# Optimization experiments

Hardware: AMD Instinct MI355X
Metric: run time of the kernel (lower is better)

## Reference

```python
import jax, jax.numpy as jnp
import numpy as np

N = 50000      # nodes
E = 800000     # edges in normalized A (incl. self loops)
DIN = 128      # input_dim
DOUT = 64      # output_dim
BN_EPS = 1e-5
SLOPE = 0.01   # LeakyReLU default negative slope


def setup_inputs() -> dict:
    key = jax.random.key(0)
    ks = jax.random.split(key, 10)
    H = jax.random.normal(ks[0], (N, DIN), dtype=jnp.float32)
    rows = jax.random.randint(ks[1], (E,), 0, N, dtype=jnp.int32)
    cols = jax.random.randint(ks[2], (E,), 0, N, dtype=jnp.int32)
    # values of the symmetrically normalized adjacency (precomputed in __init__)
    vals = jax.random.uniform(ks[3], (E,), dtype=jnp.float32)
    # BatchNorm1d params/buffers (eval mode: use running stats)
    gamma = 1.0 + 0.1 * jax.random.normal(ks[4], (DIN,), dtype=jnp.float32)
    beta = 0.1 * jax.random.normal(ks[5], (DIN,), dtype=jnp.float32)
    run_mean = 0.1 * jax.random.normal(ks[6], (DIN,), dtype=jnp.float32)
    run_var = 0.5 + jax.random.uniform(ks[7], (DIN,), dtype=jnp.float32)
    # Linear(input_dim, output_dim)
    W = jax.random.normal(ks[8], (DIN, DOUT), dtype=jnp.float32) / np.sqrt(DIN)
    b = 0.01 * jax.random.normal(ks[9], (DOUT,), dtype=jnp.float32)
    return dict(H=H, rows=rows, cols=cols, vals=vals, gamma=gamma, beta=beta,
                run_mean=run_mean, run_var=run_var, W=W, b=b)


def reference(H, rows, cols, vals, gamma, beta, run_mean, run_var, W, b):
    # F.normalize: L2 row normalization with eps=1e-12
    norm = jnp.maximum(jnp.linalg.norm(H, axis=1, keepdims=True), 1e-12)
    Hn = H / norm
    # BatchNorm1d (eval: running stats); dropout is identity in eval
    scale = gamma * jax.lax.rsqrt(run_var + BN_EPS)
    Hb = (Hn - run_mean) * scale + beta
    # Linear projection [N, DIN] @ [DIN, DOUT]
    X = Hb @ W + b
    # SpMM: out[r] = sum_{e: rows[e]==r} vals[e] * X[cols[e]]
    msgs = vals[:, None] * X[cols]            # [E, DOUT] gather + scale
    out = jax.ops.segment_sum(msgs, rows, num_segments=N)
    # LeakyReLU
    return jnp.where(out >= 0, out, SLOPE * out)
```

## Files before the change

### kernel.cpp

```cpp
#include <hip/hip_runtime.h>
#include <hip/hip_fp16.h>

#define N_NODES 50000
#define E_EDGES 800000
#define DIN 128
#define DOUT 64
#define NBUK 196
#define BUKCAP 4608
#define CHUNK 2048
#define NBLKA 391
#define NGRP 1563
#define GCAP 704
#define ASTRIDE 136

typedef short short8 __attribute__((ext_vector_type(8)));
typedef float f32x4 __attribute__((ext_vector_type(4)));

static __device__ __forceinline__ short f2bf(float f)
{
    union { float f; unsigned u; } x{f};
    const unsigned r = x.u + 0x7FFFu + ((x.u >> 16) & 1u);
    return (short)(r >> 16);
}

__global__ __launch_bounds__(256) void k_x(
    const float* __restrict__ H, const float* __restrict__ gamma,
    const float* __restrict__ beta, const float* __restrict__ mean,
    const float* __restrict__ var, const float* __restrict__ W,
    const float* __restrict__ bias, unsigned short* __restrict__ X16,
    int* __restrict__ gcursor)
{
    __shared__ short A_s[64][ASTRIDE];
    __shared__ short B_s[64][ASTRIDE];
    const int t = threadIdx.x;
    const int l = t & 63, wv = t >> 6;
    const int R0 = blockIdx.x * 64;

    if (blockIdx.x == 0 && t < NBUK) gcursor[t] = 0;

    {
        const int n = t >> 2, koff = (t & 3) * 32;
#pragma unroll
        for (int i = 0; i < 16; ++i) {
            const int k = koff + i * 2;
            const unsigned lo = (unsigned short)f2bf(W[k * DOUT + n]);
            const unsigned hi = (unsigned short)f2bf(W[(k + 1) * DOUT + n]);
            *(unsigned*)&B_s[n][k] = lo | (hi << 16);
        }
    }
    {
        const int rloc = t >> 2, sub = t & 3;
        const int r = R0 + rloc;
        float4 h[8];
        if (r < N_NODES) {
            const float4* hp = (const float4*)(H + (size_t)r * DIN + sub * 32);
#pragma unroll
            for (int i = 0; i < 8; ++i) h[i] = hp[i];
        } else {
#pragma unroll
            for (int i = 0; i < 8; ++i) h[i] = make_float4(0.f, 0.f, 0.f, 0.f);
        }
        float ss = 0.f;
#pragma unroll
        for (int i = 0; i < 8; ++i)
            ss += h[i].x * h[i].x + h[i].y * h[i].y + h[i].z * h[i].z + h[i].w * h[i].w;
        ss += __shfl_xor(ss, 1, 64);
        ss += __shfl_xor(ss, 2, 64);
        const float inv = 1.0f / fmaxf(sqrtf(ss), 1e-12f);

        const float4* gp = (const float4*)(gamma + sub * 32);
        const float4* bp = (const float4*)(beta  + sub * 32);
        const float4* mp = (const float4*)(mean  + sub * 32);
        const float4* vp = (const float4*)(var   + sub * 32);
#pragma unroll
        for (int i = 0; i < 8; ++i) {
            const float4 g4 = gp[i], b4 = bp[i], m4 = mp[i], v4 = vp[i];
            const float s0 = g4.x * rsqrtf(v4.x + 1e-5f);
            const float s1 = g4.y * rsqrtf(v4.y + 1e-5f);
            const float s2 = g4.z * rsqrtf(v4.z + 1e-5f);
            const float s3 = g4.w * rsqrtf(v4.w + 1e-5f);
            const float e0 = h[i].x * inv * s0 + (b4.x - m4.x * s0);
            const float e1 = h[i].y * inv * s1 + (b4.y - m4.y * s1);
            const float e2 = h[i].z * inv * s2 + (b4.z - m4.z * s2);
            const float e3 = h[i].w * inv * s3 + (b4.w - m4.w * s3);
            const unsigned u0 = (unsigned short)f2bf(e0) | ((unsigned)(unsigned short)f2bf(e1) << 16);
            const unsigned u1 = (unsigned short)f2bf(e2) | ((unsigned)(unsigned short)f2bf(e3) << 16);
            *(uint2*)&A_s[rloc][sub * 32 + i * 4] = make_uint2(u0, u1);
        }
    }

    const int ml = l & 15, q = l >> 4;
    f32x4 c0, c1, c2, c3;
    {
        const float b0 = bias[ml],      b1 = bias[16 + ml];
        const float b2 = bias[32 + ml], b3 = bias[48 + ml];
        c0 = f32x4{b0, b0, b0, b0};
        c1 = f32x4{b1, b1, b1, b1};
        c2 = f32x4{b2, b2, b2, b2};
        c3 = f32x4{b3, b3, b3, b3};
    }
    __syncthreads();

#pragma unroll
    for (int k0 = 0; k0 < 4; ++k0) {
        const short8 a  = *(const short8*)&A_s[wv * 16 + ml][k0 * 32 + q * 8];
        const short8 b0 = *(const short8*)&B_s[ml][k0 * 32 + q * 8];
        const short8 b1 = *(const short8*)&B_s[16 + ml][k0 * 32 + q * 8];
        const short8 b2 = *(const short8*)&B_s[32 + ml][k0 * 32 + q * 8];
        const short8 b3 = *(const short8*)&B_s[48 + ml][k0 * 32 + q * 8];
        c0 = __builtin_amdgcn_mfma_f32_16x16x32_bf16(a, b0, c0, 0, 0, 0);
        c1 = __builtin_amdgcn_mfma_f32_16x16x32_bf16(a, b1, c1, 0, 0, 0);
        c2 = __builtin_amdgcn_mfma_f32_16x16x32_bf16(a, b2, c2, 0, 0, 0);
        c3 = __builtin_amdgcn_mfma_f32_16x16x32_bf16(a, b3, c3, 0, 0, 0);
    }

    __syncthreads();
    unsigned short* otile = (unsigned short*)&A_s[0][0];
#pragma unroll
    for (int i = 0; i < 4; ++i) {
        const int r = wv * 16 + q * 4 + i;
        otile[r * 64 + ml]      = __half_as_ushort(__float2half(c0[i]));
        otile[r * 64 + 16 + ml] = __half_as_ushort(__float2half(c1[i]));
        otile[r * 64 + 32 + ml] = __half_as_ushort(__float2half(c2[i]));
        otile[r * 64 + 48 + ml] = __half_as_ushort(__float2half(c3[i]));
    }
    __syncthreads();
#pragma unroll
    for (int rep = 0; rep < 2; ++rep) {
        const int id = rep * 256 + t;
        const int row = id >> 3;
        const int off = (id & 7) * 8;
        if (R0 + row < N_NODES)
            *(uint4*)(X16 + (size_t)(R0 + row) * DOUT + off) =
                *(const uint4*)&otile[row * 64 + off];
    }
}

__global__ __launch_bounds__(512) void k_passA(
    const int* __restrict__ rows, const int* __restrict__ cols,
    const float* __restrict__ vals, int* __restrict__ gcursor,
    unsigned* __restrict__ midVC, unsigned char* __restrict__ midR)
{
    __shared__ int lhist[NBUK], lstart[NBUK], lcur[NBUK], gbase[NBUK];
    __shared__ int wsumS[4];
    __shared__ unsigned lbinVC[CHUNK];
    __shared__ unsigned short lbinBR[CHUNK];
    const int t = threadIdx.x;
    const int lane = t & 63, wv = t >> 6;
    const int e0 = blockIdx.x * CHUNK;
    const int nC = min(CHUNK, E_EDGES - e0);

    if (t < NBUK) lhist[t] = 0;
    __syncthreads();

    unsigned prVC[4];
    unsigned short prBR[4];
#pragma unroll
    for (int k = 0; k < 4; ++k) {
        const int e = e0 + k * 512 + t;
        if (e < E_EDGES) {
            const int r = rows[e];
            const unsigned hv = __half_as_ushort(__float2half(vals[e]));
            prVC[k] = (hv << 16) | (unsigned)cols[e];
            prBR[k] = (unsigned short)r;
            atomicAdd(&lhist[r >> 8], 1);
        } else {
            prBR[k] = 0xFFFFu;
        }
    }
    __syncthreads();

    const int v = (t < NBUK) ? lhist[t] : 0;
    int x = v;
    if (t < 256) {
#pragma unroll
        for (int o = 1; o < 64; o <<= 1) {
            const int y = __shfl_up(x, o, 64);
            if (lane >= o) x += y;
        }
        if (lane == 63) wsumS[wv] = x;
    }
    __syncthreads();
    if (t < NBUK) {
        int pre = 0;
        for (int i = 0; i < wv; ++i) pre += wsumS[i];
        const int ex = pre + x - v;
        lstart[t] = ex;
        lcur[t] = ex;
        gbase[t] = t * BUKCAP + (v ? atomicAdd(&gcursor[t], v) : 0);
    }
    __syncthreads();

#pragma unroll
    for (int k = 0; k < 4; ++k) {
        if (prBR[k] != 0xFFFFu) {
            const int bk = prBR[k] >> 8;
            const int pos = atomicAdd(&lcur[bk], 1);
            lbinVC[pos] = prVC[k];
            lbinBR[pos] = prBR[k];
        }
    }
    __syncthreads();

    for (int i = t; i < nC; i += 512) {
        const unsigned short br = lbinBR[i];
        const int bk = br >> 8;
        const int g = gbase[bk] + (i - lstart[bk]);
        if (g < (bk + 1) * BUKCAP) {
            midVC[g] = lbinVC[i];
            midR[g] = (unsigned char)(br & 255);
        }
    }
}

__global__ __launch_bounds__(256) void k_passB(
    const int* __restrict__ gcursor, const unsigned* __restrict__ midVC,
    const unsigned char* __restrict__ midR, unsigned* __restrict__ ev,
    int2* __restrict__ rowSE)
{
    __shared__ int lhist[32], lcur[32];
    const int g  = blockIdx.x;
    const int bk = g >> 3;
    const int q  = g & 7;
    const int base = bk * BUKCAP;
    const int total = min(gcursor[bk], BUKCAP);
    const int t = threadIdx.x;

    if (t < 32) lhist[t] = 0;
    __syncthreads();
    for (int i = t; i < total; i += 256) {
        const int lr = midR[base + i];
        if ((lr >> 5) == q) atomicAdd(&lhist[lr & 31], 1);
    }
    __syncthreads();
    if (t < 32) {
        const int v = lhist[t];
        int x = v;
#pragma unroll
        for (int o = 1; o < 32; o <<= 1) {
            const int y = __shfl_up(x, o, 64);
            if (t >= o) x += y;
        }
        const int ex = x - v;
        lcur[t] = min(ex, GCAP);
        const int row = (g << 5) | t;
        if (row < N_NODES)
            rowSE[row] = make_int2(g * GCAP + min(ex, GCAP),
                                   g * GCAP + min(ex + v, GCAP));
    }
    __syncthreads();
    for (int i = t; i < total; i += 256) {
        const int lr = midR[base + i];
        if ((lr >> 5) == q) {
            const int pos = atomicAdd(&lcur[lr & 31], 1);
            if (pos < GCAP) ev[g * GCAP + pos] = midVC[base + i];
        }
    }
}

__global__ __launch_bounds__(256) void k_spmm(
    const int2* __restrict__ rowSE, const unsigned* __restrict__ ev,
    const unsigned short* __restrict__ X16, float* __restrict__ out)
{
    const int lane = threadIdx.x & 63;
    const int ql   = lane & 15;
    const int qh   = lane >> 4;
    const int row  = blockIdx.x * 4 + (threadIdx.x >> 6);
    const int2 se = rowSE[row];
    const int s = se.x, e2 = se.y;
    float a0 = 0.f, a1 = 0.f, a2 = 0.f, a3 = 0.f;
    for (int c = s; c < e2; c += 64) {
        const int idx = c + lane;
        unsigned p = 0;
        if (idx < e2) p = ev[idx];
        const int cnt  = min(e2 - c, 64);
        const int jmax = (cnt + 3) >> 2;
        int j = 0;
        for (; j + 1 < jmax; j += 2) {
            const unsigned u0 = (unsigned)__shfl((int)p, 4 * j + qh,     64);
            const unsigned u1 = (unsigned)__shfl((int)p, 4 * j + 4 + qh, 64);
            const uint2 x0 = *(const uint2*)(X16 + (u0 & 0xFFFFu) * DOUT + 4 * ql);
            const uint2 x1 = *(const uint2*)(X16 + (u1 & 0xFFFFu) * DOUT + 4 * ql);
            const float v0 = __half2float(__ushort_as_half((unsigned short)(u0 >> 16)));
            const float v1 = __half2float(__ushort_as_half((unsigned short)(u1 >> 16)));
            const float2 f00 = __half22float2(*(const __half2*)&x0.x);
            const float2 f01 = __half22float2(*(const __half2*)&x0.y);
            const float2 f10 = __half22float2(*(const __half2*)&x1.x);
            const float2 f11 = __half22float2(*(const __half2*)&x1.y);
            a0 = fmaf(v0, f00.x, a0); a1 = fmaf(v0, f00.y, a1);
            a2 = fmaf(v0, f01.x, a2); a3 = fmaf(v0, f01.y, a3);
            a0 = fmaf(v1, f10.x, a0); a1 = fmaf(v1, f10.y, a1);
            a2 = fmaf(v1, f11.x, a2); a3 = fmaf(v1, f11.y, a3);
        }
        for (; j < jmax; ++j) {
            const unsigned u = (unsigned)__shfl((int)p, 4 * j + qh, 64);
            const uint2 xx = *(const uint2*)(X16 + (u & 0xFFFFu) * DOUT + 4 * ql);
            const float v = __half2float(__ushort_as_half((unsigned short)(u >> 16)));
            const float2 f0 = __half22float2(*(const __half2*)&xx.x);
            const float2 f1 = __half22float2(*(const __half2*)&xx.y);
            a0 = fmaf(v, f0.x, a0); a1 = fmaf(v, f0.y, a1);
            a2 = fmaf(v, f1.x, a2); a3 = fmaf(v, f1.y, a3);
        }
    }
    a0 += __shfl_xor(a0, 16, 64); a0 += __shfl_xor(a0, 32, 64);
    a1 += __shfl_xor(a1, 16, 64); a1 += __shfl_xor(a1, 32, 64);
    a2 += __shfl_xor(a2, 16, 64); a2 += __shfl_xor(a2, 32, 64);
    a3 += __shfl_xor(a3, 16, 64); a3 += __shfl_xor(a3, 32, 64);
    if (lane < 16) {
        float4 r;
        r.x = (a0 >= 0.f) ? a0 : 0.01f * a0;
        r.y = (a1 >= 0.f) ? a1 : 0.01f * a1;
        r.z = (a2 >= 0.f) ? a2 : 0.01f * a2;
        r.w = (a3 >= 0.f) ? a3 : 0.01f * a3;
        *(float4*)(out + (size_t)row * DOUT + 4 * ql) = r;
    }
}

extern "C" void kernel_launch(void* const* d_in, const int* in_sizes, int n_in,
                              void* d_out, int out_size, void* d_ws, size_t ws_size,
                              hipStream_t stream)
{
    const float* H     = (const float*)d_in[0];
    const int*   rows  = (const int*)  d_in[1];
    const int*   cols  = (const int*)  d_in[2];
    const float* vals  = (const float*)d_in[3];
    const float* gamma = (const float*)d_in[4];
    const float* beta  = (const float*)d_in[5];
    const float* mean  = (const float*)d_in[6];
    const float* var   = (const float*)d_in[7];
    const float* W     = (const float*)d_in[8];
    const float* bias  = (const float*)d_in[9];
    float* out = (float*)d_out;

    char* ws = (char*)d_ws;
    unsigned short* X16     = (unsigned short*)(ws);
    int*            gcursor = (int*)          (ws +  6400000);
    unsigned*       midVC   = (unsigned*)     (ws +  6400800);
    unsigned char*  midR    = (unsigned char*)(ws + 10013472);
    unsigned*       ev      = (unsigned*)     (ws + 10916640);
    int2*           rowSE   = (int2*)         (ws + 15318048);

    k_x<<<(N_NODES + 63) / 64, 256, 0, stream>>>(H, gamma, beta, mean, var, W,
                                                 bias, X16, gcursor);
    k_passA<<<NBLKA, 512, 0, stream>>>(rows, cols, vals, gcursor, midVC, midR);
    k_passB<<<NGRP, 256, 0, stream>>>(gcursor, midVC, midR, ev, rowSE);
    k_spmm<<<N_NODES / 4, 256, 0, stream>>>(rowSE, ev, X16, out);
}
```

Measured before the change: 160.6 us.

## Fuse row-bucketing pass with SpMM using LDS atomic accumulation per 32-row group

Replaces the second bucketing pass and the per-row SpMM kernel with one kernel per 32-row group. Each group compacts its matching edges into shared memory with a wave-ballot queue, then gathers X rows and accumulates with shared-memory float atomics into a padded 32x64 tile. LeakyReLU is applied when the tile is written out. This removes one launch and the global round trip through the ev and rowSE buffers. In exchange it relies on LDS atomics, whose contention may be high, and float summation order is no longer deterministic.

```diff
diff --git a/kernel.cpp b/kernel.cpp
--- a/kernel.cpp
+++ b/kernel.cpp
@@ -10,7 +10,7 @@
 #define CHUNK 2048
 #define NBLKA 391
 #define NGRP 1563
-#define GCAP 704
+#define QCAP 768
 #define ASTRIDE 136
 
 typedef short short8 __attribute__((ext_vector_type(8)));
@@ -213,106 +213,76 @@
     }
 }
 
-__global__ __launch_bounds__(256) void k_passB(
+__global__ __launch_bounds__(256) void k_spmmf(
     const int* __restrict__ gcursor, const unsigned* __restrict__ midVC,
-    const unsigned char* __restrict__ midR, unsigned* __restrict__ ev,
-    int2* __restrict__ rowSE)
-{
-    __shared__ int lhist[32], lcur[32];
-    const int g  = blockIdx.x;
+    const unsigned char* __restrict__ midR, const unsigned short* __restrict__ X16,
+    float* __restrict__ out)
+{
+    __shared__ float acc[32 * 65];
+    __shared__ unsigned qVC[QCAP];
+    __shared__ int qR[QCAP];
+    __shared__ int qcount;
+    const int t = threadIdx.x;
+    const int g = blockIdx.x;
     const int bk = g >> 3;
     const int q  = g & 7;
     const int base = bk * BUKCAP;
     const int total = min(gcursor[bk], BUKCAP);
-    const int t = threadIdx.x;
-
-    if (t < 32) lhist[t] = 0;
-    __syncthreads();
-    for (int i = t; i < total; i += 256) {
-        const int lr = midR[base + i];
-        if ((lr >> 5) == q) atomicAdd(&lhist[lr & 31], 1);
-    }
-    __syncthreads();
-    if (t < 32) {
-        const int v = lhist[t];
-        int x = v;
-#pragma unroll
-        for (int o = 1; o < 32; o <<= 1) {
-            const int y = __shfl_up(x, o, 64);
-            if (t >= o) x += y;
-        }
-        const int ex = x - v;
-        lcur[t] = min(ex, GCAP);
-        const int row = (g << 5) | t;
-        if (row < N_NODES)
-            rowSE[row] = make_int2(g * GCAP + min(ex, GCAP),
-                                   g * GCAP + min(ex + v, GCAP));
-    }
-    __syncthreads();
-    for (int i = t; i < total; i += 256) {
-        const int lr = midR[base + i];
-        if ((lr >> 5) == q) {
-            const int pos = atomicAdd(&lcur[lr & 31], 1);
-            if (pos < GCAP) ev[g * GCAP + pos] = midVC[base + i];
-        }
-    }
-}
-
-__global__ __launch_bounds__(256) void k_spmm(
-    const int2* __restrict__ rowSE, const unsigned* __restrict__ ev,
-    const unsigned short* __restrict__ X16, float* __restrict__ out)
-{
-    const int lane = threadIdx.x & 63;
-    const int ql   = lane & 15;
-    const int qh   = lane >> 4;
-    const int row  = blockIdx.x * 4 + (threadIdx.x >> 6);
-    const int2 se = rowSE[row];
-    const int s = se.x, e2 = se.y;
-    float a0 = 0.f, a1 = 0.f, a2 = 0.f, a3 = 0.f;
-    for (int c = s; c < e2; c += 64) {
-        const int idx = c + lane;
-        unsigned p = 0;
-        if (idx < e2) p = ev[idx];
-        const int cnt  = min(e2 - c, 64);
-        const int jmax = (cnt + 3) >> 2;
-        int j = 0;
-        for (; j + 1 < jmax; j += 2) {
-            const unsigned u0 = (unsigned)__shfl((int)p, 4 * j + qh,     64);
-            const unsigned u1 = (unsigned)__shfl((int)p, 4 * j + 4 + qh, 64);
-            const uint2 x0 = *(const uint2*)(X16 + (u0 & 0xFFFFu) * DOUT + 4 * ql);
-            const uint2 x1 = *(const uint2*)(X16 + (u1 & 0xFFFFu) * DOUT + 4 * ql);
-            const float v0 = __half2float(__ushort_as_half((unsigned short)(u0 >> 16)));
-            const float v1 = __half2float(__ushort_as_half((unsigned short)(u1 >> 16)));
-            const float2 f00 = __half22float2(*(const __half2*)&x0.x);
-            const float2 f01 = __half22float2(*(const __half2*)&x0.y);
-            const float2 f10 = __half22float2(*(const __half2*)&x1.x);
-            const float2 f11 = __half22float2(*(const __half2*)&x1.y);
-            a0 = fmaf(v0, f00.x, a0); a1 = fmaf(v0, f00.y, a1);
-            a2 = fmaf(v0, f01.x, a2); a3 = fmaf(v0, f01.y, a3);
-            a0 = fmaf(v1, f10.x, a0); a1 = fmaf(v1, f10.y, a1);
-            a2 = fmaf(v1, f11.x, a2); a3 = fmaf(v1, f11.y, a3);
-        }
-        for (; j < jmax; ++j) {
-            const unsigned u = (unsigned)__shfl((int)p, 4 * j + qh, 64);
-            const uint2 xx = *(const uint2*)(X16 + (u & 0xFFFFu) * DOUT + 4 * ql);
-            const float v = __half2float(__ushort_as_half((unsigned short)(u >> 16)));
-            const float2 f0 = __half22float2(*(const __half2*)&xx.x);
-            const float2 f1 = __half22float2(*(const __half2*)&xx.y);
-            a0 = fmaf(v, f0.x, a0); a1 = fmaf(v, f0.y, a1);
-            a2 = fmaf(v, f1.x, a2); a3 = fmaf(v, f1.y, a3);
-        }
-    }
-    a0 += __shfl_xor(a0, 16, 64); a0 += __shfl_xor(a0, 32, 64);
-    a1 += __shfl_xor(a1, 16, 64); a1 += __shfl_xor(a1, 32, 64);
-    a2 += __shfl_xor(a2, 16, 64); a2 += __shfl_xor(a2, 32, 64);
-    a3 += __shfl_xor(a3, 16, 64); a3 += __shfl_xor(a3, 32, 64);
-    if (lane < 16) {
-        float4 r;
-        r.x = (a0 >= 0.f) ? a0 : 0.01f * a0;
-        r.y = (a1 >= 0.f) ? a1 : 0.01f * a1;
-        r.z = (a2 >= 0.f) ? a2 : 0.01f * a2;
-        r.w = (a3 >= 0.f) ? a3 : 0.01f * a3;
-        *(float4*)(out + (size_t)row * DOUT + 4 * ql) = r;
+    const int lane = t & 63;
+
+    for (int i = t; i < 32 * 65; i += 256) acc[i] = 0.f;
+    if (t == 0) qcount = 0;
+    __syncthreads();
+
+    for (int i0 = t; i0 < total; i0 += 256) {
+        const int lr = midR[base + i0];
+        const bool match = (lr >> 5) == q;
+        const unsigned long long m = __ballot(match);
+        if (m) {
+            const int ldr = (int)(__ffsll((long long)m) - 1);
+            const int pre = __popcll(m & ((1ull << lane) - 1ull));
+            int bs = 0;
+            if (lane == ldr) bs = atomicAdd(&qcount, __popcll(m));
+            bs = __shfl(bs, ldr, 64);
+            if (match) {
+                const int pos = bs + pre;
+                if (pos < QCAP) {
+                    qVC[pos] = midVC[base + i0];
+                    qR[pos]  = lr & 31;
+                }
+            }
+        }
+    }
+    __syncthreads();
+    const int qc = min(qcount, QCAP);
+
+    const int grp = t >> 4;
+    const int ql  = t & 15;
+    for (int i = grp; i < qc; i += 16) {
+        const unsigned vc = qVC[i];
+        const int rl = qR[i];
+        const float v = __half2float(__ushort_as_half((unsigned short)(vc >> 16)));
+        const uint2 x = *(const uint2*)(X16 + (size_t)(vc & 0xFFFFu) * DOUT + 4 * ql);
+        const float2 f0 = __half22float2(*(const __half2*)&x.x);
+        const float2 f1 = __half22float2(*(const __half2*)&x.y);
+        float* ap = &acc[rl * 65 + 4 * ql];
+        atomicAdd(ap + 0, v * f0.x);
+        atomicAdd(ap + 1, v * f0.y);
+        atomicAdd(ap + 2, v * f1.x);
+        atomicAdd(ap + 3, v * f1.y);
+    }
+    __syncthreads();
+
+    const int r0 = g << 5;
+#pragma unroll
+    for (int k = 0; k < 8; ++k) {
+        const int id = k * 256 + t;
+        const int r = id >> 6, c = id & 63;
+        if (r0 + r < N_NODES) {
+            float a = acc[r * 65 + c];
+            a = (a >= 0.f) ? a : 0.01f * a;
+            out[(size_t)(r0 + r) * DOUT + c] = a;
+        }
     }
 }
 
@@ -337,12 +307,9 @@
     int*            gcursor = (int*)          (ws +  6400000);
     unsigned*       midVC   = (unsigned*)     (ws +  6400800);
     unsigned char*  midR    = (unsigned char*)(ws + 10013472);
-    unsigned*       ev      = (unsigned*)     (ws + 10916640);
-    int2*           rowSE   = (int2*)         (ws + 15318048);
 
     k_x<<<(N_NODES + 63) / 64, 256, 0, stream>>>(H, gamma, beta, mean, var, W,
                                                  bias, X16, gcursor);
     k_passA<<<NBLKA, 512, 0, stream>>>(rows, cols, vals, gcursor, midVC, midR);
-    k_passB<<<NGRP, 256, 0, stream>>>(gcursor, midVC, midR, ev, rowSE);
-    k_spmm<<<N_NODES / 4, 256, 0, stream>>>(rowSE, ev, X16, out);
-}
+    k_spmmf<<<NGRP, 256, 0, stream>>>(gcursor, midVC, midR, X16, out);
+}
```

Result: slower. 434.7 us (+170.6%).

## Merge feature projection and edge binning into one launch; narrow SpMM gather

Applied to the files above, without the earlier changes.

Fuses the dense projection kernel and the first edge-bucketing pass into a single launch. Blocks are dispatched by block index to either role, so the two independent stages run concurrently and one launch is saved. The gcursor reset moves to a hipMemsetAsync, which adds a small operation. Separately, the SpMM kernel now processes two edges per iteration, with 32 lanes each loading 4 bytes, instead of four edges with 16 lanes each loading 8 bytes. This trades load width against the number of shuffle reductions.

```diff
diff --git a/kernel.cpp b/kernel.cpp
--- a/kernel.cpp
+++ b/kernel.cpp
@@ -9,9 +9,11 @@
 #define BUKCAP 4608
 #define CHUNK 2048
 #define NBLKA 391
+#define NXP 391
 #define NGRP 1563
 #define GCAP 704
 #define ASTRIDE 136
+#define TILEB (64 * ASTRIDE * 2)
 
 typedef short short8 __attribute__((ext_vector_type(8)));
 typedef float f32x4 __attribute__((ext_vector_type(4)));
@@ -23,192 +25,197 @@
     return (short)(r >> 16);
 }
 
-__global__ __launch_bounds__(256) void k_x(
+__global__ __launch_bounds__(512) void k_xa(
     const float* __restrict__ H, const float* __restrict__ gamma,
     const float* __restrict__ beta, const float* __restrict__ mean,
     const float* __restrict__ var, const float* __restrict__ W,
     const float* __restrict__ bias, unsigned short* __restrict__ X16,
-    int* __restrict__ gcursor)
-{
-    __shared__ short A_s[64][ASTRIDE];
-    __shared__ short B_s[64][ASTRIDE];
-    const int t = threadIdx.x;
-    const int l = t & 63, wv = t >> 6;
-    const int R0 = blockIdx.x * 64;
-
-    if (blockIdx.x == 0 && t < NBUK) gcursor[t] = 0;
-
-    {
-        const int n = t >> 2, koff = (t & 3) * 32;
-#pragma unroll
-        for (int i = 0; i < 16; ++i) {
-            const int k = koff + i * 2;
-            const unsigned lo = (unsigned short)f2bf(W[k * DOUT + n]);
-            const unsigned hi = (unsigned short)f2bf(W[(k + 1) * DOUT + n]);
-            *(unsigned*)&B_s[n][k] = lo | (hi << 16);
-        }
-    }
-    {
-        const int rloc = t >> 2, sub = t & 3;
-        const int r = R0 + rloc;
-        float4 h[8];
-        if (r < N_NODES) {
-            const float4* hp = (const float4*)(H + (size_t)r * DIN + sub * 32);
-#pragma unroll
-            for (int i = 0; i < 8; ++i) h[i] = hp[i];
-        } else {
-#pragma unroll
-            for (int i = 0; i < 8; ++i) h[i] = make_float4(0.f, 0.f, 0.f, 0.f);
-        }
-        float ss = 0.f;
-#pragma unroll
-        for (int i = 0; i < 8; ++i)
-            ss += h[i].x * h[i].x + h[i].y * h[i].y + h[i].z * h[i].z + h[i].w * h[i].w;
-        ss += __shfl_xor(ss, 1, 64);
-        ss += __shfl_xor(ss, 2, 64);
-        const float inv = 1.0f / fmaxf(sqrtf(ss), 1e-12f);
-
-        const float4* gp = (const float4*)(gamma + sub * 32);
-        const float4* bp = (const float4*)(beta  + sub * 32);
-        const float4* mp = (const float4*)(mean  + sub * 32);
-        const float4* vp = (const float4*)(var   + sub * 32);
-#pragma unroll
-        for (int i = 0; i < 8; ++i) {
-            const float4 g4 = gp[i], b4 = bp[i], m4 = mp[i], v4 = vp[i];
-            const float s0 = g4.x * rsqrtf(v4.x + 1e-5f);
-            const float s1 = g4.y * rsqrtf(v4.y + 1e-5f);
-            const float s2 = g4.z * rsqrtf(v4.z + 1e-5f);
-            const float s3 = g4.w * rsqrtf(v4.w + 1e-5f);
-            const float e0 = h[i].x * inv * s0 + (b4.x - m4.x * s0);
-            const float e1 = h[i].y * inv * s1 + (b4.y - m4.y * s1);
-            const float e2 = h[i].z * inv * s2 + (b4.z - m4.z * s2);
-            const float e3 = h[i].w * inv * s3 + (b4.w - m4.w * s3);
-            const unsigned u0 = (unsigned short)f2bf(e0) | ((unsigned)(unsigned short)f2bf(e1) << 16);
-            const unsigned u1 = (unsigned short)f2bf(e2) | ((unsigned)(unsigned short)f2bf(e3) << 16);
-            *(uint2*)&A_s[rloc][sub * 32 + i * 4] = make_uint2(u0, u1);
-        }
-    }
-
-    const int ml = l & 15, q = l >> 4;
-    f32x4 c0, c1, c2, c3;
-    {
-        const float b0 = bias[ml],      b1 = bias[16 + ml];
-        const float b2 = bias[32 + ml], b3 = bias[48 + ml];
-        c0 = f32x4{b0, b0, b0, b0};
-        c1 = f32x4{b1, b1, b1, b1};
-        c2 = f32x4{b2, b2, b2, b2};
-        c3 = f32x4{b3, b3, b3, b3};
-    }
-    __syncthreads();
-
-#pragma unroll
-    for (int k0 = 0; k0 < 4; ++k0) {
-        const short8 a  = *(const short8*)&A_s[wv * 16 + ml][k0 * 32 + q * 8];
-        const short8 b0 = *(const short8*)&B_s[ml][k0 * 32 + q * 8];
-        const short8 b1 = *(const short8*)&B_s[16 + ml][k0 * 32 + q * 8];
-        const short8 b2 = *(const short8*)&B_s[32 + ml][k0 * 32 + q * 8];
-        const short8 b3 = *(const short8*)&B_s[48 + ml][k0 * 32 + q * 8];
-        c0 = __builtin_amdgcn_mfma_f32_16x16x32_bf16(a, b0, c0, 0, 0, 0);
-        c1 = __builtin_amdgcn_mfma_f32_16x16x32_bf16(a, b1, c1, 0, 0, 0);
-        c2 = __builtin_amdgcn_mfma_f32_16x16x32_bf16(a, b2, c2, 0, 0, 0);
-        c3 = __builtin_amdgcn_mfma_f32_16x16x32_bf16(a, b3, c3, 0, 0, 0);
-    }
-
-    __syncthreads();
-    unsigned short* otile = (unsigned short*)&A_s[0][0];
-#pragma unroll
-    for (int i = 0; i < 4; ++i) {
-        const int r = wv * 16 + q * 4 + i;
-        otile[r * 64 + ml]      = __half_as_ushort(__float2half(c0[i]));
-        otile[r * 64 + 16 + ml] = __half_as_ushort(__float2half(c1[i]));
-        otile[r * 64 + 32 + ml] = __half_as_ushort(__float2half(c2[i]));
-        otile[r * 64 + 48 + ml] = __half_as_ushort(__float2half(c3[i]));
-    }
-    __syncthreads();
-#pragma unroll
-    for (int rep = 0; rep < 2; ++rep) {
-        const int id = rep * 256 + t;
-        const int row = id >> 3;
-        const int off = (id & 7) * 8;
-        if (R0 + row < N_NODES)
-            *(uint4*)(X16 + (size_t)(R0 + row) * DOUT + off) =
-                *(const uint4*)&otile[row * 64 + off];
-    }
-}
-
-__global__ __launch_bounds__(512) void k_passA(
     const int* __restrict__ rows, const int* __restrict__ cols,
     const float* __restrict__ vals, int* __restrict__ gcursor,
     unsigned* __restrict__ midVC, unsigned char* __restrict__ midR)
 {
-    __shared__ int lhist[NBUK], lstart[NBUK], lcur[NBUK], gbase[NBUK];
-    __shared__ int wsumS[4];
-    __shared__ unsigned lbinVC[CHUNK];
-    __shared__ unsigned short lbinBR[CHUNK];
+    __shared__ __align__(16) char smem[2][TILEB * 2];
+    const int bid = blockIdx.x;
     const int t = threadIdx.x;
-    const int lane = t & 63, wv = t >> 6;
-    const int e0 = blockIdx.x * CHUNK;
-    const int nC = min(CHUNK, E_EDGES - e0);
-
-    if (t < NBUK) lhist[t] = 0;
-    __syncthreads();
-
-    unsigned prVC[4];
-    unsigned short prBR[4];
-#pragma unroll
-    for (int k = 0; k < 4; ++k) {
-        const int e = e0 + k * 512 + t;
-        if (e < E_EDGES) {
-            const int r = rows[e];
-            const unsigned hv = __half_as_ushort(__float2half(vals[e]));
-            prVC[k] = (hv << 16) | (unsigned)cols[e];
-            prBR[k] = (unsigned short)r;
-            atomicAdd(&lhist[r >> 8], 1);
-        } else {
-            prBR[k] = 0xFFFFu;
-        }
-    }
-    __syncthreads();
-
-    const int v = (t < NBUK) ? lhist[t] : 0;
-    int x = v;
-    if (t < 256) {
-#pragma unroll
-        for (int o = 1; o < 64; o <<= 1) {
-            const int y = __shfl_up(x, o, 64);
-            if (lane >= o) x += y;
-        }
-        if (lane == 63) wsumS[wv] = x;
-    }
-    __syncthreads();
-    if (t < NBUK) {
-        int pre = 0;
-        for (int i = 0; i < wv; ++i) pre += wsumS[i];
-        const int ex = pre + x - v;
-        lstart[t] = ex;
-        lcur[t] = ex;
-        gbase[t] = t * BUKCAP + (v ? atomicAdd(&gcursor[t], v) : 0);
-    }
-    __syncthreads();
-
-#pragma unroll
-    for (int k = 0; k < 4; ++k) {
-        if (prBR[k] != 0xFFFFu) {
-            const int bk = prBR[k] >> 8;
-            const int pos = atomicAdd(&lcur[bk], 1);
-            lbinVC[pos] = prVC[k];
-            lbinBR[pos] = prBR[k];
-        }
-    }
-    __syncthreads();
-
-    for (int i = t; i < nC; i += 512) {
-        const unsigned short br = lbinBR[i];
-        const int bk = br >> 8;
-        const int g = gbase[bk] + (i - lstart[bk]);
-        if (g < (bk + 1) * BUKCAP) {
-            midVC[g] = lbinVC[i];
-            midR[g] = (unsigned char)(br & 255);
+
+    if (bid < NBLKA) {
+        int* lhist  = (int*)smem[0];
+        int* lstart = lhist + 256;
+        int* lcur   = lstart + 256;
+        int* gbase  = lcur + 256;
+        int* wsumS  = gbase + 256;
+        unsigned* lbinVC = (unsigned*)(wsumS + 16);
+        unsigned short* lbinBR = (unsigned short*)(lbinVC + CHUNK);
+
+        const int lane = t & 63, wv = t >> 6;
+        const int e0 = bid * CHUNK;
+        const int nC = min(CHUNK, E_EDGES - e0);
+
+        if (t < NBUK) lhist[t] = 0;
+        __syncthreads();
+
+        unsigned prVC[4];
+        unsigned short prBR[4];
+#pragma unroll
+        for (int k = 0; k < 4; ++k) {
+            const int e = e0 + k * 512 + t;
+            if (e < E_EDGES) {
+                const int r = rows[e];
+                const unsigned hv = __half_as_ushort(__float2half(vals[e]));
+                prVC[k] = (hv << 16) | (unsigned)cols[e];
+                prBR[k] = (unsigned short)r;
+                atomicAdd(&lhist[r >> 8], 1);
+            } else {
+                prBR[k] = 0xFFFFu;
+            }
+        }
+        __syncthreads();
+
+        const int v = (t < NBUK) ? lhist[t] : 0;
+        int x = v;
+        if (t < 256) {
+#pragma unroll
+            for (int o = 1; o < 64; o <<= 1) {
+                const int y = __shfl_up(x, o, 64);
+                if (lane >= o) x += y;
+            }
+            if (lane == 63) wsumS[wv] = x;
+        }
+        __syncthreads();
+        if (t < NBUK) {
+            int pre = 0;
+            for (int i = 0; i < wv; ++i) pre += wsumS[i];
+            const int ex = pre + x - v;
+            lstart[t] = ex;
+            lcur[t] = ex;
+            gbase[t] = t * BUKCAP + (v ? atomicAdd(&gcursor[t], v) : 0);
+        }
+        __syncthreads();
+
+#pragma unroll
+        for (int k = 0; k < 4; ++k) {
+            if (prBR[k] != 0xFFFFu) {
+                const int bk = prBR[k] >> 8;
+                const int pos = atomicAdd(&lcur[bk], 1);
+                lbinVC[pos] = prVC[k];
+                lbinBR[pos] = prBR[k];
+            }
+        }
+        __syncthreads();
+
+        for (int i = t; i < nC; i += 512) {
+            const unsigned short br = lbinBR[i];
+            const int bk = br >> 8;
+            const int g = gbase[bk] + (i - lstart[bk]);
+            if (g < (bk + 1) * BUKCAP) {
+                midVC[g] = lbinVC[i];
+                midR[g] = (unsigned char)(br & 255);
+            }
+        }
+    } else {
+        const int pair = bid - NBLKA;
+        const int tile = t >> 8;
+        const int tt = t & 255;
+        short (*A_s)[ASTRIDE] = (short(*)[ASTRIDE])(smem[tile]);
+        short (*B_s)[ASTRIDE] = (short(*)[ASTRIDE])(smem[tile] + TILEB);
+        const int l = tt & 63, wv = tt >> 6;
+        const int R0 = (pair * 2 + tile) * 64;
+
+        {
+            const int n = tt >> 2, koff = (tt & 3) * 32;
+#pragma unroll
+            for (int i = 0; i < 16; ++i) {
+                const int k = koff + i * 2;
+                const unsigned lo = (unsigned short)f2bf(W[k * DOUT + n]);
+                const unsigned hi = (unsigned short)f2bf(W[(k + 1) * DOUT + n]);
+                *(unsigned*)&B_s[n][k] = lo | (hi << 16);
+            }
+        }
+        {
+            const int rloc = tt >> 2, sub = tt & 3;
+            const int r = R0 + rloc;
+            float4 h[8];
+            if (r < N_NODES) {
+                const float4* hp = (const float4*)(H + (size_t)r * DIN + sub * 32);
+#pragma unroll
+                for (int i = 0; i < 8; ++i) h[i] = hp[i];
+            } else {
+#pragma unroll
+                for (int i = 0; i < 8; ++i) h[i] = make_float4(0.f, 0.f, 0.f, 0.f);
+            }
+            float ss = 0.f;
+#pragma unroll
+            for (int i = 0; i < 8; ++i)
+                ss += h[i].x * h[i].x + h[i].y * h[i].y + h[i].z * h[i].z + h[i].w * h[i].w;
+            ss += __shfl_xor(ss, 1, 64);
+            ss += __shfl_xor(ss, 2, 64);
+            const float inv = 1.0f / fmaxf(sqrtf(ss), 1e-12f);
+
+            const float4* gp = (const float4*)(gamma + sub * 32);
+            const float4* bp = (const float4*)(beta  + sub * 32);
+            const float4* mp = (const float4*)(mean  + sub * 32);
+            const float4* vp = (const float4*)(var   + sub * 32);
+#pragma unroll
+            for (int i = 0; i < 8; ++i) {
+                const float4 g4 = gp[i], b4 = bp[i], m4 = mp[i], v4 = vp[i];
+                const float s0 = g4.x * rsqrtf(v4.x + 1e-5f);
+                const float s1 = g4.y * rsqrtf(v4.y + 1e-5f);
+                const float s2 = g4.z * rsqrtf(v4.z + 1e-5f);
+                const float s3 = g4.w * rsqrtf(v4.w + 1e-5f);
+                const float e0 = h[i].x * inv * s0 + (b4.x - m4.x * s0);
+                const float e1 = h[i].y * inv * s1 + (b4.y - m4.y * s1);
+                const float e2 = h[i].z * inv * s2 + (b4.z - m4.z * s2);
+                const float e3 = h[i].w * inv * s3 + (b4.w - m4.w * s3);
+                const unsigned u0 = (unsigned short)f2bf(e0) | ((unsigned)(unsigned short)f2bf(e1) << 16);
+                const unsigned u1 = (unsigned short)f2bf(e2) | ((unsigned)(unsigned short)f2bf(e3) << 16);
+                *(uint2*)&A_s[rloc][sub * 32 + i * 4] = make_uint2(u0, u1);
+            }
+        }
+
+        const int ml = l & 15, q = l >> 4;
+        f32x4 c0, c1, c2, c3;
+        {
+            const float b0 = bias[ml],      b1 = bias[16 + ml];
+            const float b2 = bias[32 + ml], b3 = bias[48 + ml];
+            c0 = f32x4{b0, b0, b0, b0};
+            c1 = f32x4{b1, b1, b1, b1};
+            c2 = f32x4{b2, b2, b2, b2};
+            c3 = f32x4{b3, b3, b3, b3};
+        }
+        __syncthreads();
+
+#pragma unroll
+        for (int k0 = 0; k0 < 4; ++k0) {
+            const short8 a  = *(const short8*)&A_s[wv * 16 + ml][k0 * 32 + q * 8];
+            const short8 b0 = *(const short8*)&B_s[ml][k0 * 32 + q * 8];
+            const short8 b1 = *(const short8*)&B_s[16 + ml][k0 * 32 + q * 8];
+            const short8 b2 = *(const short8*)&B_s[32 + ml][k0 * 32 + q * 8];
+            const short8 b3 = *(const short8*)&B_s[48 + ml][k0 * 32 + q * 8];
+            c0 = __builtin_amdgcn_mfma_f32_16x16x32_bf16(a, b0, c0, 0, 0, 0);
+            c1 = __builtin_amdgcn_mfma_f32_16x16x32_bf16(a, b1, c1, 0, 0, 0);
+            c2 = __builtin_amdgcn_mfma_f32_16x16x32_bf16(a, b2, c2, 0, 0, 0);
+            c3 = __builtin_amdgcn_mfma_f32_16x16x32_bf16(a, b3, c3, 0, 0, 0);
+        }
+
+        __syncthreads();
+        unsigned short* otile = (unsigned short*)&A_s[0][0];
+#pragma unroll
+        for (int i = 0; i < 4; ++i) {
+            const int r = wv * 16 + q * 4 + i;
+            otile[r * 64 + ml]      = __half_as_ushort(__float2half(c0[i]));
+            otile[r * 64 + 16 + ml] = __half_as_ushort(__float2half(c1[i]));
+            otile[r * 64 + 32 + ml] = __half_as_ushort(__float2half(c2[i]));
+            otile[r * 64 + 48 + ml] = __half_as_ushort(__float2half(c3[i]));
+        }
+        __syncthreads();
+#pragma unroll
+        for (int rep = 0; rep < 2; ++rep) {
+            const int id = rep * 256 + tt;
+            const int row = id >> 3;
+            const int off = (id & 7) * 8;
+            if (R0 + row < N_NODES)
+                *(uint4*)(X16 + (size_t)(R0 + row) * DOUT + off) =
+                    *(const uint4*)&otile[row * 64 + off];
         }
     }
 }
@@ -263,56 +270,46 @@
     const unsigned short* __restrict__ X16, float* __restrict__ out)
 {
     const int lane = threadIdx.x & 63;
-    const int ql   = lane & 15;
-    const int qh   = lane >> 4;
+    const int hl   = lane & 31;
+    const int h    = lane >> 5;
     const int row  = blockIdx.x * 4 + (threadIdx.x >> 6);
     const int2 se = rowSE[row];
     const int s = se.x, e2 = se.y;
-    float a0 = 0.f, a1 = 0.f, a2 = 0.f, a3 = 0.f;
+    float ax = 0.f, ay = 0.f;
     for (int c = s; c < e2; c += 64) {
         const int idx = c + lane;
         unsigned p = 0;
         if (idx < e2) p = ev[idx];
         const int cnt  = min(e2 - c, 64);
-        const int jmax = (cnt + 3) >> 2;
+        const int jmax = (cnt + 1) >> 1;
         int j = 0;
         for (; j + 1 < jmax; j += 2) {
-            const unsigned u0 = (unsigned)__shfl((int)p, 4 * j + qh,     64);
-            const unsigned u1 = (unsigned)__shfl((int)p, 4 * j + 4 + qh, 64);
-            const uint2 x0 = *(const uint2*)(X16 + (u0 & 0xFFFFu) * DOUT + 4 * ql);
-            const uint2 x1 = *(const uint2*)(X16 + (u1 & 0xFFFFu) * DOUT + 4 * ql);
+            const unsigned u0 = (unsigned)__shfl((int)p, 2 * j + h,     64);
+            const unsigned u1 = (unsigned)__shfl((int)p, 2 * j + 2 + h, 64);
+            const unsigned x0 = *(const unsigned*)(X16 + (u0 & 0xFFFFu) * DOUT + 2 * hl);
+            const unsigned x1 = *(const unsigned*)(X16 + (u1 & 0xFFFFu) * DOUT + 2 * hl);
             const float v0 = __half2float(__ushort_as_half((unsigned short)(u0 >> 16)));
             const float v1 = __half2float(__ushort_as_half((unsigned short)(u1 >> 16)));
-            const float2 f00 = __half22float2(*(const __half2*)&x0.x);
-            const float2 f01 = __half22float2(*(const __half2*)&x0.y);
-            const float2 f10 = __half22float2(*(const __half2*)&x1.x);
-            const float2 f11 = __half22float2(*(const __half2*)&x1.y);
-            a0 = fmaf(v0, f00.x, a0); a1 = fmaf(v0, f00.y, a1);
-            a2 = fmaf(v0, f01.x, a2); a3 = fmaf(v0, f01.y, a3);
-            a0 = fmaf(v1, f10.x, a0); a1 = fmaf(v1, f10.y, a1);
-            a2 = fmaf(v1, f11.x, a2); a3 = fmaf(v1, f11.y, a3);
+            const float2 f0 = __half22float2(*(const __half2*)&x0);
+            const float2 f1 = __half22float2(*(const __half2*)&x1);
+            ax = fmaf(v0, f0.x, ax); ay = fmaf(v0, f0.y, ay);
+            ax = fmaf(v1, f1.x, ax); ay = fmaf(v1, f1.y, ay);
         }
         for (; j < jmax; ++j) {
-            const unsigned u = (unsigned)__shfl((int)p, 4 * j + qh, 64);
-            const uint2 xx = *(const uint2*)(X16 + (u & 0xFFFFu) * DOUT + 4 * ql);
+            const unsigned u = (unsigned)__shfl((int)p, 2 * j + h, 64);
+            const unsigned x = *(const unsigned*)(X16 + (u & 0xFFFFu) * DOUT + 2 * hl);
             const float v = __half2float(__ushort_as_half((unsigned short)(u >> 16)));
-            const float2 f0 = __half22float2(*(const __half2*)&xx.x);
-            const float2 f1 = __half22float2(*(const __half2*)&xx.y);
-            a0 = fmaf(v, f0.x, a0); a1 = fmaf(v, f0.y, a1);
-            a2 = fmaf(v, f1.x, a2); a3 = fmaf(v, f1.y, a3);
-        }
-    }
-    a0 += __shfl_xor(a0, 16, 64); a0 += __shfl_xor(a0, 32, 64);
-    a1 += __shfl_xor(a1, 16, 64); a1 += __shfl_xor(a1, 32, 64);
-    a2 += __shfl_xor(a2, 16, 64); a2 += __shfl_xor(a2, 32, 64);
-    a3 += __shfl_xor(a3, 16, 64); a3 += __shfl_xor(a3, 32, 64);
-    if (lane < 16) {
-        float4 r;
-        r.x = (a0 >= 0.f) ? a0 : 0.01f * a0;
-        r.y = (a1 >= 0.f) ? a1 : 0.01f * a1;
-        r.z = (a2 >= 0.f) ? a2 : 0.01f * a2;
-        r.w = (a3 >= 0.f) ? a3 : 0.01f * a3;
-        *(float4*)(out + (size_t)row * DOUT + 4 * ql) = r;
+            const float2 f = __half22float2(*(const __half2*)&x);
+            ax = fmaf(v, f.x, ax); ay = fmaf(v, f.y, ay);
+        }
+    }
+    ax += __shfl_xor(ax, 32, 64);
+    ay += __shfl_xor(ay, 32, 64);
+    if (h == 0) {
+        float2 r;
+        r.x = (ax >= 0.f) ? ax : 0.01f * ax;
+        r.y = (ay >= 0.f) ? ay : 0.01f * ay;
+        *(float2*)(out + (size_t)row * DOUT + 2 * hl) = r;
     }
 }
 
@@ -340,9 +337,10 @@
     unsigned*       ev      = (unsigned*)     (ws + 10916640);
     int2*           rowSE   = (int2*)         (ws + 15318048);
 
-    k_x<<<(N_NODES + 63) / 64, 256, 0, stream>>>(H, gamma, beta, mean, var, W,
-                                                 bias, X16, gcursor);
-    k_passA<<<NBLKA, 512, 0, stream>>>(rows, cols, vals, gcursor, midVC, midR);
+    hipMemsetAsync(gcursor, 0, NBUK * sizeof(int), stream);
+    k_xa<<<NBLKA + NXP, 512, 0, stream>>>(H, gamma, beta, mean, var, W, bias,
+                                          X16, rows, cols, vals, gcursor,
+                                          midVC, midR);
     k_passB<<<NGRP, 256, 0, stream>>>(gcursor, midVC, midR, ev, rowSE);
     k_spmm<<<N_NODES / 4, 256, 0, stream>>>(rowSE, ev, X16, out);
 }
```

Result: slower. 165.8 us (+3.2%).
